# Kernel optimization log

Hardware: AMD Instinct MI355X
Metric: run time of the kernel (lower is better)

Reference implementation:

```python
import jax, jax.numpy as jnp
import numpy as np

EPS = 1e-5
G, N, H, P, K = 8, 128, 64, 64, 4  # n_groups, d_state, n_heads, head_dim, conv kernel
R = H // G  # heads per group


def _rmsnorm(x, w, eps=EPS):
    return x * jax.lax.rsqrt(jnp.mean(x * x, axis=-1, keepdims=True) + eps) * w


def setup_inputs() -> dict:
    key = jax.random.key(0)
    ks = jax.random.split(key, 8)
    B, L, Dm = 2, 1024, 2048
    d_inner = 2 * Dm                      # 4096
    conv_dim = d_inner + 2 * G * N        # 6144
    proj_dim = 2 * d_inner + 2 * G * N + H  # 10304
    return {
        "hidden_states": jax.random.normal(ks[0], (B, L, Dm), jnp.float32),
        "residual": jax.random.normal(ks[1], (B, L, Dm), jnp.float32),
        "norm_w": jnp.ones((Dm,), jnp.float32),
        "in_proj_w": jax.random.normal(ks[2], (proj_dim, Dm), jnp.float32) * 0.02,
        "conv_w": jax.random.normal(ks[3], (conv_dim, K), jnp.float32) * 0.1,
        "conv_b": jnp.zeros((conv_dim,), jnp.float32),
        "A_log": jnp.log(jnp.arange(1, H + 1, dtype=jnp.float32)),
        "D_param": jnp.ones((H,), jnp.float32),
        "dt_bias": jax.random.uniform(ks[4], (H,), jnp.float32, -4.0, -1.0),
        "gate_norm_w": jnp.ones((d_inner,), jnp.float32),
        "out_proj_w": jax.random.normal(ks[5], (Dm, d_inner), jnp.float32) * 0.02,
    }


def reference(hidden_states, residual, norm_w, in_proj_w, conv_w, conv_b,
              A_log, D_param, dt_bias, gate_norm_w, out_proj_w):
    B, L, Dm = hidden_states.shape
    d_inner = 2 * Dm
    conv_dim = d_inner + 2 * G * N

    # fused residual-add RMSNorm (residual is not None branch)
    h = hidden_states + residual
    new_residual = h
    x = _rmsnorm(h, norm_w)

    # in_proj -> [z | xBC | dt]
    proj = jnp.einsum('bld,ed->ble', x, in_proj_w)
    z = proj[..., :d_inner]
    xBC = proj[..., d_inner:d_inner + conv_dim]
    dt = proj[..., d_inner + conv_dim:]            # [B, L, H]

    # causal depthwise conv1d over xBC, then SiLU
    lhs = jnp.transpose(xBC, (0, 2, 1))            # [B, C, L]
    rhs = conv_w[:, None, :]                       # [C, 1, K]
    conv = jax.lax.conv_general_dilated(
        lhs, rhs, window_strides=(1,), padding=[(K - 1, 0)],
        feature_group_count=conv_dim)
    xBC = jax.nn.silu(jnp.transpose(conv, (0, 2, 1)) + conv_b)

    xs = xBC[..., :d_inner].reshape(B, L, G, R, P)   # per-head inputs
    Bm = xBC[..., d_inner:d_inner + G * N].reshape(B, L, G, N)
    Cm = xBC[..., d_inner + G * N:].reshape(B, L, G, N)

    dt = jax.nn.softplus(dt + dt_bias)               # [B, L, H]
    A = -jnp.exp(A_log)                              # [H]
    dA = jnp.exp(dt * A).reshape(B, L, G, R)
    dtg = dt.reshape(B, L, G, R)

    # time-major for scan
    def step(hst, inp):
        dA_t, dt_t, x_t, B_t, C_t = inp            # [B,G,R], [B,G,R], [B,G,R,P], [B,G,N], [B,G,N]
        dBx = jnp.einsum('bgr,bgn,bgrp->bgrpn', dt_t, B_t, x_t)
        hst = hst * dA_t[..., None, None] + dBx    # [B,G,R,P,N]
        y_t = jnp.einsum('bgrpn,bgn->bgrp', hst, C_t)
        return hst, y_t

    tm = lambda a: jnp.moveaxis(a, 1, 0)
    h0 = jnp.zeros((B, G, R, P, N), hidden_states.dtype)
    _, ys = jax.lax.scan(step, h0, (tm(dA), tm(dtg), tm(xs), tm(Bm), tm(Cm)))
    y = jnp.moveaxis(ys, 0, 1)                     # [B, L, G, R, P]
    y = y + D_param.reshape(G, R)[None, None, :, :, None] * xs
    y = y.reshape(B, L, d_inner)

    # gated RMSNorm then out_proj
    y = _rmsnorm(y * jax.nn.silu(z), gate_norm_w)
    out = jnp.einsum('ble,de->bld', y, out_proj_w)
    return out, new_residual
```

## Files before the change

kernel.cpp:

```cpp
#include <hip/hip_runtime.h>

#define TOK 2048
#define DM 2048
#define DI 4096
#define NG 8
#define NN 128
#define PROJ_D 10304
#define PROJ_P 10496
#define CONV_D 6144
#define LSEQ 1024
#define CHUNK 64
#define NCHUNK 16

typedef unsigned short u16;
typedef __attribute__((ext_vector_type(4))) float f32x4;
typedef __attribute__((ext_vector_type(8))) short s16x8;
typedef __attribute__((ext_vector_type(4))) unsigned short u16x4;

__device__ __forceinline__ u16 f2bf(float f) {
  union { float f; unsigned u; } x; x.f = f;
  unsigned r = (x.u + 0x7FFFu + ((x.u >> 16) & 1u)) >> 16;
  return (u16)r;
}
__device__ __forceinline__ float bf2f(u16 u) {
  union { unsigned u; float f; } x; x.u = ((unsigned)u) << 16; return x.f;
}

__device__ __forceinline__ float blockReduceSum256(float s) {
  __shared__ float red[4];
  #pragma unroll
  for (int o = 32; o > 0; o >>= 1) s += __shfl_down(s, o, 64);
  int lane = threadIdx.x & 63, wid = threadIdx.x >> 6;
  if (lane == 0) red[wid] = s;
  __syncthreads();
  return red[0] + red[1] + red[2] + red[3];
}

__global__ __launch_bounds__(256) void cvt_bf16_pad(const float* __restrict__ src, u16* __restrict__ dst,
                                                    long n_src, long n_dst) {
  long i = ((long)blockIdx.x * 256 + threadIdx.x) * 4;
  if (i >= n_dst) return;
  u16x4 o;
  if (i < n_src) {
    f32x4 v = *(const f32x4*)&src[i];
    o.x = f2bf(v.x); o.y = f2bf(v.y); o.z = f2bf(v.z); o.w = f2bf(v.w);
  } else {
    o.x = 0; o.y = 0; o.z = 0; o.w = 0;
  }
  *(u16x4*)&dst[i] = o;
}

__global__ __launch_bounds__(256) void addnorm_kernel(const float* __restrict__ hs, const float* __restrict__ res,
        const float* __restrict__ w, float* __restrict__ nres, u16* __restrict__ xbf) {
  int row = blockIdx.x;
  size_t base = (size_t)row * DM;
  int tid = threadIdx.x;
  f32x4 h[2];
  float s = 0.f;
  #pragma unroll
  for (int i = 0; i < 2; i++) {
    int off = i * 1024 + tid * 4;
    f32x4 a = *(const f32x4*)&hs[base + off];
    f32x4 b = *(const f32x4*)&res[base + off];
    f32x4 v = a + b;
    h[i] = v;
    *(f32x4*)&nres[base + off] = v;
    s += v.x * v.x + v.y * v.y + v.z * v.z + v.w * v.w;
  }
  s = blockReduceSum256(s);
  float rs = rsqrtf(s * (1.f / DM) + 1e-5f);
  #pragma unroll
  for (int i = 0; i < 2; i++) {
    int off = i * 1024 + tid * 4;
    f32x4 wv = *(const f32x4*)&w[off];
    f32x4 v = h[i];
    u16x4 o;
    o.x = f2bf(v.x * rs * wv.x);
    o.y = f2bf(v.y * rs * wv.y);
    o.z = f2bf(v.z * rs * wv.z);
    o.w = f2bf(v.w * rs * wv.w);
    *(u16x4*)&xbf[base + off] = o;
  }
}

__device__ __forceinline__ void gld_lds16(const void* g, void* l) {
  __builtin_amdgcn_global_load_lds((const __attribute__((address_space(1))) void*)g,
                                   (__attribute__((address_space(3))) void*)l, 16, 0, 0);
}

__global__ __launch_bounds__(512, 2) void gemm8p(const u16* __restrict__ A, const u16* __restrict__ Bw,
                                                 u16* __restrict__ C, int K, int Cstride, int nbx) {
  __shared__ u16 As[2][256][64];
  __shared__ u16 Bs[2][256][64];
  int tid = threadIdx.x;
  int lane = tid & 63, w = tid >> 6;
  int wr = w >> 2, wc = w & 3;
  int cpx = gridDim.x >> 3;
  int bid = blockIdx.x;
  int lb = (bid & 7) * cpx + (bid >> 3);
  int by = lb / nbx, bx = lb - by * nbx;
  size_t m0 = (size_t)by * 256, n0 = (size_t)bx * 256;
  const u16* Ab = A + m0 * K;
  const u16* Bb = Bw + n0 * K;

  f32x4 acc[8][4];
  #pragma unroll
  for (int i = 0; i < 8; ++i)
    #pragma unroll
    for (int j = 0; j < 4; ++j) acc[i][j] = (f32x4){0.f, 0.f, 0.f, 0.f};

  int l3 = lane >> 3;
  int colsw = ((lane & 7) ^ l3) << 3;
  int fr = lane & 15, fq = lane >> 4;
  int pc0 = (fq * 8) ^ ((fr & 7) << 3);
  int pc1 = pc0 ^ 32;

  auto S = [&](int kt, int mat, int half) {
    int d = kt & 1;
    const u16* src = mat ? Bb : Ab;
    u16* dstbase = mat ? &Bs[d][0][0] : &As[d][0][0];
    #pragma unroll
    for (int j = 0; j < 2; ++j) {
      int rb = half * 128 + (w * 2 + j) * 8;
      gld_lds16(src + (size_t)(rb + l3) * K + kt * 64 + colsw, dstbase + rb * 64);
    }
  };

  int nkt = K >> 6;
  S(0, 1, 0); S(0, 1, 1); S(0, 0, 0); S(0, 0, 1);
  S(1, 1, 0); S(1, 1, 1);
  asm volatile("s_waitcnt vmcnt(4)" ::: "memory");
  __builtin_amdgcn_s_barrier();

  for (int kt = 0; kt < nkt; ++kt) {
    int d = kt & 1;
    s16x8 b[4][2];
    #pragma unroll
    for (int q = 0; q < 4; ++q) {
      if (q == 0) {
        #pragma unroll
        for (int ni = 0; ni < 4; ++ni) {
          b[ni][0] = *(const s16x8*)&Bs[d][wc * 64 + ni * 16 + fr][pc0];
          b[ni][1] = *(const s16x8*)&Bs[d][wc * 64 + ni * 16 + fr][pc1];
        }
      }
      s16x8 a[2][2];
      #pragma unroll
      for (int mi = 0; mi < 2; ++mi) {
        a[mi][0] = *(const s16x8*)&As[d][wr * 128 + q * 32 + mi * 16 + fr][pc0];
        a[mi][1] = *(const s16x8*)&As[d][wr * 128 + q * 32 + mi * 16 + fr][pc1];
      }
      if (q == 0)      { if (kt + 1 < nkt) S(kt + 1, 0, 0); }
      else if (q == 1) { if (kt + 1 < nkt) S(kt + 1, 0, 1); }
      else if (q == 2) { if (kt + 2 < nkt) S(kt + 2, 1, 0); }
      else {
        if (kt + 2 < nkt) { S(kt + 2, 1, 1); asm volatile("s_waitcnt vmcnt(4)" ::: "memory"); }
        else              { asm volatile("s_waitcnt vmcnt(0)" ::: "memory"); }
      }
      __builtin_amdgcn_s_barrier();
      __builtin_amdgcn_s_setprio(1);
      #pragma unroll
      for (int mi = 0; mi < 2; ++mi)
        #pragma unroll
        for (int ni = 0; ni < 4; ++ni) {
          acc[q * 2 + mi][ni] = __builtin_amdgcn_mfma_f32_16x16x32_bf16(a[mi][0], b[ni][0], acc[q * 2 + mi][ni], 0, 0, 0);
          acc[q * 2 + mi][ni] = __builtin_amdgcn_mfma_f32_16x16x32_bf16(a[mi][1], b[ni][1], acc[q * 2 + mi][ni], 0, 0, 0);
        }
      __builtin_amdgcn_s_setprio(0);
      __builtin_amdgcn_s_barrier();
    }
  }
  size_t crow0 = m0 + wr * 128 + fq * 4;
  size_t ccol0 = n0 + wc * 64 + fr;
  #pragma unroll
  for (int mf = 0; mf < 8; ++mf)
    #pragma unroll
    for (int ni = 0; ni < 4; ++ni)
      #pragma unroll
      for (int j = 0; j < 4; ++j)
        C[(crow0 + mf * 16 + j) * Cstride + ccol0 + ni * 16] = f2bf(acc[mf][ni][j]);
}

template <int BM, int BN>
__global__ __launch_bounds__((BM / 64) * (BN / 64) * 64, 2)
void gemm_pipe(const u16* __restrict__ A, const u16* __restrict__ Bw,
               float* __restrict__ C, int K, int Cstride, int nbx) {
  constexpr int WM = BM / 64, WN = BN / 64;
  constexpr int NA = 8 / WN;
  constexpr int NB = 8 / WM;
  constexpr int NV = NA + NB;
  __shared__ u16 As[2][BM][64];
  __shared__ u16 Bs[2][BN][64];
  int tid = threadIdx.x;
  int lane = tid & 63, w = tid >> 6;
  int wr = w / WN, wc = w % WN;
  int cpx = gridDim.x >> 3;
  int bid = blockIdx.x;
  int lb = (bid & 7) * cpx + (bid >> 3);
  int by = lb / nbx, bx = lb - by * nbx;
  size_t m0 = (size_t)by * BM, n0 = (size_t)bx * BN;
  const u16* Ab = A + m0 * K;
  const u16* Bb = Bw + n0 * K;

  f32x4 acc[4][4];
  #pragma unroll
  for (int i = 0; i < 4; ++i)
    #pragma unroll
    for (int j = 0; j < 4; ++j) acc[i][j] = (f32x4){0.f, 0.f, 0.f, 0.f};

  int l3 = lane >> 3;
  int colsw = ((lane & 7) ^ l3) << 3;
  int fr = lane & 15, fq = lane >> 4;
  int pc0 = (fq * 8) ^ ((fr & 7) << 3);
  int pc1 = pc0 ^ 32;

  auto STAGE = [&](int d, int kt) {
    #pragma unroll
    for (int j = 0; j < NA; ++j) {
      int row = wr * 64 + (wc * NA + j) * 8;
      gld_lds16(Ab + (size_t)(row + l3) * K + kt * 64 + colsw, &As[d][row][0]);
    }
    #pragma unroll
    for (int j = 0; j < NB; ++j) {
      int row = wc * 64 + (wr * NB + j) * 8;
      gld_lds16(Bb + (size_t)(row + l3) * K + kt * 64 + colsw, &Bs[d][row][0]);
    }
  };

  int nkt = K >> 6;
  STAGE(0, 0);
  for (int kt = 0; kt < nkt; ++kt) {
    int d = kt & 1, nd = d ^ 1;
    if (kt + 1 < nkt) {
      STAGE(nd, kt + 1);
      if constexpr (NV == 6) asm volatile("s_waitcnt vmcnt(6)" ::: "memory");
      else                   asm volatile("s_waitcnt vmcnt(8)" ::: "memory");
    } else {
      asm volatile("s_waitcnt vmcnt(0)" ::: "memory");
    }
    __builtin_amdgcn_s_barrier();
    s16x8 b[4][2];
    #pragma unroll
    for (int ni = 0; ni < 4; ++ni) {
      b[ni][0] = *(const s16x8*)&Bs[d][wc * 64 + ni * 16 + fr][pc0];
      b[ni][1] = *(const s16x8*)&Bs[d][wc * 64 + ni * 16 + fr][pc1];
    }
    {
      s16x8 a[2][2];
      #pragma unroll
      for (int mi = 0; mi < 2; ++mi) {
        a[mi][0] = *(const s16x8*)&As[d][wr * 64 + mi * 16 + fr][pc0];
        a[mi][1] = *(const s16x8*)&As[d][wr * 64 + mi * 16 + fr][pc1];
      }
      __builtin_amdgcn_s_setprio(1);
      #pragma unroll
      for (int mi = 0; mi < 2; ++mi)
        #pragma unroll
        for (int ni = 0; ni < 4; ++ni) {
          acc[mi][ni] = __builtin_amdgcn_mfma_f32_16x16x32_bf16(a[mi][0], b[ni][0], acc[mi][ni], 0, 0, 0);
          acc[mi][ni] = __builtin_amdgcn_mfma_f32_16x16x32_bf16(a[mi][1], b[ni][1], acc[mi][ni], 0, 0, 0);
        }
      __builtin_amdgcn_s_setprio(0);
    }
    __builtin_amdgcn_s_barrier();
    {
      s16x8 a[2][2];
      #pragma unroll
      for (int mi = 0; mi < 2; ++mi) {
        a[mi][0] = *(const s16x8*)&As[d][wr * 64 + (mi + 2) * 16 + fr][pc0];
        a[mi][1] = *(const s16x8*)&As[d][wr * 64 + (mi + 2) * 16 + fr][pc1];
      }
      __builtin_amdgcn_s_setprio(1);
      #pragma unroll
      for (int mi = 0; mi < 2; ++mi)
        #pragma unroll
        for (int ni = 0; ni < 4; ++ni) {
          acc[mi + 2][ni] = __builtin_amdgcn_mfma_f32_16x16x32_bf16(a[mi][0], b[ni][0], acc[mi + 2][ni], 0, 0, 0);
          acc[mi + 2][ni] = __builtin_amdgcn_mfma_f32_16x16x32_bf16(a[mi][1], b[ni][1], acc[mi + 2][ni], 0, 0, 0);
        }
      __builtin_amdgcn_s_setprio(0);
    }
    __builtin_amdgcn_s_barrier();
  }
  size_t crow0 = m0 + wr * 64 + fq * 4;
  size_t ccol0 = n0 + wc * 64 + fr;
  #pragma unroll
  for (int mi = 0; mi < 4; ++mi)
    #pragma unroll
    for (int ni = 0; ni < 4; ++ni)
      #pragma unroll
      for (int j = 0; j < 4; ++j)
        C[(crow0 + mi * 16 + j) * Cstride + ccol0 + ni * 16] = acc[mi][ni][j];
}

__global__ __launch_bounds__(256) void conv_silu_kernel(const u16* __restrict__ proj,
        const float* __restrict__ cw, const float* __restrict__ cb, u16* __restrict__ xbc) {
  long gid = (long)blockIdx.x * 256 + threadIdx.x;
  int c4 = (int)(gid % 1536);
  long t = gid / 1536;
  int l = (int)(t & 1023);
  int c = c4 * 4;
  const u16* base = proj + (size_t)t * PROJ_P + DI + c;
  f32x4 acc = *(const f32x4*)&cb[c];
  f32x4 w0 = *(const f32x4*)&cw[(c + 0) * 4];
  f32x4 w1 = *(const f32x4*)&cw[(c + 1) * 4];
  f32x4 w2 = *(const f32x4*)&cw[(c + 2) * 4];
  f32x4 w3 = *(const f32x4*)&cw[(c + 3) * 4];
  #pragma unroll
  for (int k = 0; k < 4; k++) {
    int ls = l - 3 + k;
    if (ls >= 0) {
      u16x4 v = *(const u16x4*)(base + ((long)(k - 3)) * PROJ_P);
      acc.x = fmaf(bf2f(v.x), w0[k], acc.x);
      acc.y = fmaf(bf2f(v.y), w1[k], acc.y);
      acc.z = fmaf(bf2f(v.z), w2[k], acc.z);
      acc.w = fmaf(bf2f(v.w), w3[k], acc.w);
    }
  }
  u16x4 o;
  o.x = f2bf(acc.x / (1.f + expf(-acc.x)));
  o.y = f2bf(acc.y / (1.f + expf(-acc.y)));
  o.z = f2bf(acc.z / (1.f + expf(-acc.z)));
  o.w = f2bf(acc.w / (1.f + expf(-acc.w)));
  *(u16x4*)&xbc[(size_t)t * CONV_D + c] = o;
}

__global__ __launch_bounds__(256) void dt_kernel(const u16* __restrict__ proj, const float* __restrict__ dt_bias,
        const float* __restrict__ A_log, float* __restrict__ dtspT, float* __restrict__ dtaT) {
  int idx = blockIdx.x * 256 + threadIdx.x;
  int t = idx >> 6, hh = idx & 63;
  int b = t >> 10, l = t & 1023;
  float dtv = bf2f(proj[(size_t)t * PROJ_P + (DI + CONV_D) + hh]) + dt_bias[hh];
  float sp = (dtv > 15.f) ? dtv : log1pf(expf(dtv));
  float Ah = -expf(A_log[hh]);
  size_t o = (size_t)(b * 64 + hh) * LSEQ + l;
  dtspT[o] = sp;
  dtaT[o] = sp * Ah;
}

__global__ __launch_bounds__(512) void ssd_kernel(const u16* __restrict__ xbc, const float* __restrict__ dtsp,
        const float* __restrict__ dta, const float* __restrict__ Dp, float* __restrict__ y) {
  int bid = blockIdx.x;
  int g = bid & 7, b = (bid >> 3) & 1, r = bid >> 4;
  int h = g * 8 + r;
  int tid = threadIdx.x;
  int w = tid >> 6, lane = tid & 63;

  __shared__ u16 Bsh[2][64][128];
  __shared__ u16 Csh[2][64][128];
  __shared__ u16 Xt[2][64][64];
  __shared__ u16 Btw[2][128][64];
  __shared__ u16 GWsh[64][64];
  __shared__ u16 Hbf[64][128];
  __shared__ float dtsh[LSEQ];
  __shared__ float Lsh[LSEQ];

  const float* dtrow = dtsp + (size_t)(b * 64 + h) * LSEQ;
  const float* dtarow = dta + (size_t)(b * 64 + h) * LSEQ;
  if (tid < 256) { f32x4 v = *(const f32x4*)&dtrow[tid * 4]; *(f32x4*)&dtsh[tid * 4] = v; }
  for (int cc = w; cc < NCHUNK; cc += 8) {
    float a = dtarow[cc * 64 + lane];
    #pragma unroll
    for (int o = 1; o < 64; o <<= 1) { float t2 = __shfl_up(a, o, 64); if (lane >= o) a += t2; }
    Lsh[cc * 64 + lane] = a;
  }
  {
    u16* hp = &Hbf[0][0];
    for (int i = tid; i < 2048; i += 512) *(u16x4*)&hp[i * 4] = (u16x4){0, 0, 0, 0};
  }
  float Dv = Dp[h];
  const u16* xb = xbc + (size_t)b * LSEQ * CONV_D;
  int swz = (lane & 7) << 3;
  __syncthreads();

  auto stage = [&](int cc, int d) {
    int t0c = cc * 64;
    int pw = w - 4, ptid = tid - 256;
    #pragma unroll
    for (int q = 0; q < 4; ++q) {
      int rowb = pw * 16 + q * 4;
      int row = rowb + (lane >> 4);
      int colb = ((lane & 15) * 8) ^ ((row & 7) << 3);
      gld_lds16(xb + (size_t)(t0c + row) * CONV_D + DI + g * 128 + colb, &Bsh[d][rowb][0]);
      gld_lds16(xb + (size_t)(t0c + row) * CONV_D + DI + NG * NN + g * 128 + colb, &Csh[d][rowb][0]);
    }
    {
      int s = ptid & 63, pq = ptid >> 6;
      const u16* xr = xb + (size_t)(t0c + s) * CONV_D + g * 512 + r * 64;
      #pragma unroll
      for (int pb = 0; pb < 4; ++pb) {
        int p0 = pb * 16 + pq * 4;
        u16x4 v = *(const u16x4*)&xr[p0];
        #pragma unroll
        for (int j = 0; j < 4; ++j) {
          int p = p0 + j;
          Xt[d][p][s ^ ((p & 7) << 3)] = v[j];
        }
      }
    }
    {
      int s = ptid & 63, nq = ptid >> 6;
      float wend = __expf(Lsh[t0c + 63] - Lsh[t0c + s]) * dtsh[t0c + s];
      const u16* br = xb + (size_t)(t0c + s) * CONV_D + DI + g * 128;
      #pragma unroll
      for (int nb = 0; nb < 8; ++nb) {
        int n0 = nb * 16 + nq * 4;
        u16x4 v = *(const u16x4*)&br[n0];
        #pragma unroll
        for (int j = 0; j < 4; ++j) {
          int n = n0 + j;
          Btw[d][n][s ^ ((n & 7) << 3)] = f2bf(bf2f(v[j]) * wend);
        }
      }
    }
  };

  if (w >= 4) stage(0, 0);
  __syncthreads();

  f32x4 hst[8];
  #pragma unroll
  for (int i = 0; i < 8; i++) hst[i] = (f32x4){0.f, 0.f, 0.f, 0.f};

  for (int c = 0; c < NCHUNK; ++c) {
    int d = c & 1;
    int t0c = c * 64;
    f32x4 Yacc[4], Y2acc[4];
    s16x8 aC[4];
    float el[4];
    if (w >= 4) {
      if (c + 1 < NCHUNK) stage(c + 1, d ^ 1);
    } else {
      #pragma unroll
      for (int k = 0; k < 4; ++k)
        aC[k] = *(const s16x8*)&Csh[d][w * 16 + (lane & 15)][(k * 32 + (lane >> 4) * 8) ^ swz];
      f32x4 Gacc[4];
      #pragma unroll
      for (int st = 0; st < 4; ++st) Gacc[st] = (f32x4){0.f, 0.f, 0.f, 0.f};
      #pragma unroll
      for (int st = 0; st < 4; ++st)
        #pragma unroll
        for (int k = 0; k < 4; ++k) {
          s16x8 bB = *(const s16x8*)&Bsh[d][st * 16 + (lane & 15)][(k * 32 + (lane >> 4) * 8) ^ swz];
          Gacc[st] = __builtin_amdgcn_mfma_f32_16x16x32_bf16(aC[k], bB, Gacc[st], 0, 0, 0);
        }
      #pragma unroll
      for (int st = 0; st < 4; ++st) {
        int s = st * 16 + (lane & 15);
        float Ls = Lsh[t0c + s], dts = dtsh[t0c + s];
        #pragma unroll
        for (int j = 0; j < 4; ++j) {
          int t = w * 16 + (lane >> 4) * 4 + j;
          float wgt = (s <= t) ? __expf(Lsh[t0c + t] - Ls) * dts : 0.f;
          GWsh[t][s ^ ((t & 7) << 3)] = f2bf(Gacc[st][j] * wgt);
        }
      }
      #pragma unroll
      for (int pt = 0; pt < 4; ++pt) { Yacc[pt] = (f32x4){0.f,0.f,0.f,0.f}; Y2acc[pt] = (f32x4){0.f,0.f,0.f,0.f}; }
      s16x8 aGW[2];
      #pragma unroll
      for (int k = 0; k < 2; ++k)
        aGW[k] = *(const s16x8*)&GWsh[w * 16 + (lane & 15)][(k * 32 + (lane >> 4) * 8) ^ swz];
      #pragma unroll
      for (int pt = 0; pt < 4; ++pt) {
        #pragma unroll
        for (int k = 0; k < 2; ++k) {
          s16x8 bX = *(const s16x8*)&Xt[d][pt * 16 + (lane & 15)][(k * 32 + (lane >> 4) * 8) ^ swz];
          Yacc[pt] = __builtin_amdgcn_mfma_f32_16x16x32_bf16(aGW[k], bX, Yacc[pt], 0, 0, 0);
        }
        #pragma unroll
        for (int k = 0; k < 4; ++k) {
          s16x8 bH = *(const s16x8*)&Hbf[pt * 16 + (lane & 15)][(k * 32 + (lane >> 4) * 8) ^ swz];
          Y2acc[pt] = __builtin_amdgcn_mfma_f32_16x16x32_bf16(aC[k], bH, Y2acc[pt], 0, 0, 0);
        }
      }
      #pragma unroll
      for (int j = 0; j < 4; ++j) el[j] = __expf(Lsh[t0c + w * 16 + (lane >> 4) * 4 + j]);
      #pragma unroll
      for (int pt = 0; pt < 4; ++pt) {
        int p = pt * 16 + (lane & 15);
        #pragma unroll
        for (int j = 0; j < 4; ++j) {
          int t = w * 16 + (lane >> 4) * 4 + j;
          float xv = bf2f(Xt[d][p][t ^ ((p & 7) << 3)]);
          float yv = Yacc[pt][j] + el[j] * Y2acc[pt][j] + Dv * xv;
          y[((size_t)b * LSEQ + t0c + t) * DI + g * 512 + r * 64 + p] = yv;
        }
      }
      float e63 = __expf(Lsh[t0c + 63]);
      s16x8 aX[2];
      #pragma unroll
      for (int k = 0; k < 2; ++k)
        aX[k] = *(const s16x8*)&Xt[d][w * 16 + (lane & 15)][(k * 32 + (lane >> 4) * 8) ^ swz];
      #pragma unroll
      for (int nt = 0; nt < 8; ++nt) {
        #pragma unroll
        for (int j = 0; j < 4; ++j) hst[nt][j] *= e63;
        #pragma unroll
        for (int k = 0; k < 2; ++k) {
          s16x8 bW = *(const s16x8*)&Btw[d][nt * 16 + (lane & 15)][(k * 32 + (lane >> 4) * 8) ^ swz];
          hst[nt] = __builtin_amdgcn_mfma_f32_16x16x32_bf16(aX[k], bW, hst[nt], 0, 0, 0);
        }
      }
    }
    __syncthreads();
    if (w < 4) {
      #pragma unroll
      for (int nt = 0; nt < 8; ++nt) {
        int n = nt * 16 + (lane & 15);
        #pragma unroll
        for (int j = 0; j < 4; ++j) {
          int p = w * 16 + (lane >> 4) * 4 + j;
          Hbf[p][n ^ ((p & 7) << 3)] = f2bf(hst[nt][j]);
        }
      }
    }
    __syncthreads();
  }
}

__global__ __launch_bounds__(256) void gate_kernel(const float* __restrict__ y, const u16* __restrict__ proj,
        const float* __restrict__ gw, u16* __restrict__ y2) {
  int row = blockIdx.x;
  const float* yr = y + (size_t)row * DI;
  const u16* zr = proj + (size_t)row * PROJ_P;
  int tid = threadIdx.x;
  f32x4 v[4];
  float s = 0.f;
  #pragma unroll
  for (int i = 0; i < 4; i++) {
    int off = i * 1024 + tid * 4;
    f32x4 a = *(const f32x4*)&yr[off];
    u16x4 zv = *(const u16x4*)&zr[off];
    f32x4 t;
    float z0 = bf2f(zv.x), z1 = bf2f(zv.y), z2 = bf2f(zv.z), z3 = bf2f(zv.w);
    t.x = a.x * (z0 / (1.f + expf(-z0)));
    t.y = a.y * (z1 / (1.f + expf(-z1)));
    t.z = a.z * (z2 / (1.f + expf(-z2)));
    t.w = a.w * (z3 / (1.f + expf(-z3)));
    v[i] = t;
    s += t.x * t.x + t.y * t.y + t.z * t.z + t.w * t.w;
  }
  s = blockReduceSum256(s);
  float rs = rsqrtf(s * (1.f / DI) + 1e-5f);
  #pragma unroll
  for (int i = 0; i < 4; i++) {
    int off = i * 1024 + tid * 4;
    f32x4 wv = *(const f32x4*)&gw[off];
    u16x4 o;
    o.x = f2bf(v[i].x * rs * wv.x);
    o.y = f2bf(v[i].y * rs * wv.y);
    o.z = f2bf(v[i].z * rs * wv.z);
    o.w = f2bf(v[i].w * rs * wv.w);
    *(u16x4*)&y2[(size_t)row * DI + off] = o;
  }
}

extern "C" void kernel_launch(void* const* d_in, const int* in_sizes, int n_in,
                              void* d_out, int out_size, void* d_ws, size_t ws_size,
                              hipStream_t stream) {
  (void)in_sizes; (void)n_in; (void)out_size; (void)ws_size;
  const float* hs      = (const float*)d_in[0];
  const float* res     = (const float*)d_in[1];
  const float* norm_w  = (const float*)d_in[2];
  const float* w_in    = (const float*)d_in[3];
  const float* conv_w  = (const float*)d_in[4];
  const float* conv_b  = (const float*)d_in[5];
  const float* A_log   = (const float*)d_in[6];
  const float* D_param = (const float*)d_in[7];
  const float* dt_bias = (const float*)d_in[8];
  const float* gate_w  = (const float*)d_in[9];
  const float* w_out   = (const float*)d_in[10];

  float* out  = (float*)d_out;
  float* nres = out + (size_t)TOK * DM;

  char* ws = (char*)d_ws;
  size_t off = 0;
  u16*   WB1  = (u16*)(ws + off);   off += (size_t)PROJ_P * DM * 2;
  u16*   WB2  = (u16*)(ws + off);   off += (size_t)DM * DI * 2;
  u16*   XBF  = (u16*)(ws + off);   off += (size_t)TOK * DM * 2;
  u16*   PROJ = (u16*)(ws + off);   off += (size_t)TOK * PROJ_P * 2;
  u16*   XBC  = (u16*)(ws + off);   off += (size_t)TOK * CONV_D * 2;
  float* DTSP = (float*)(ws + off); off += (size_t)TOK * 64 * 4;
  float* DTA  = (float*)(ws + off); off += (size_t)TOK * 64 * 4;
  float* Y    = (float*)(ws + off); off += (size_t)TOK * DI * 4;
  u16*   Y2   = (u16*)(ws + off);   off += (size_t)TOK * DI * 2;

  cvt_bf16_pad<<<20992, 256, 0, stream>>>(w_in, WB1, (long)PROJ_D * DM, (long)PROJ_P * DM);
  cvt_bf16_pad<<<8192, 256, 0, stream>>>(w_out, WB2, (long)DM * DI, (long)DM * DI);
  addnorm_kernel<<<TOK, 256, 0, stream>>>(hs, res, norm_w, nres, XBF);
  gemm8p<<<(TOK / 256) * (PROJ_P / 256), 512, 0, stream>>>(XBF, WB1, PROJ, DM, PROJ_P, PROJ_P / 256);
  conv_silu_kernel<<<(TOK * (CONV_D / 4)) / 256, 256, 0, stream>>>(PROJ, conv_w, conv_b, XBC);
  dt_kernel<<<(TOK * 64) / 256, 256, 0, stream>>>(PROJ, dt_bias, A_log, DTSP, DTA);
  ssd_kernel<<<128, 512, 0, stream>>>(XBC, DTSP, DTA, D_param, Y);
  gate_kernel<<<TOK, 256, 0, stream>>>(Y, PROJ, gate_w, Y2);
  gemm_pipe<128, 128><<<(TOK / 128) * (DM / 128), 256, 0, stream>>>(Y2, WB2, out, DI, DM, DM / 128);
}
```

Before: 336.9 us.

## Use split-K 256x256 GEMM for out_proj and store SSD output as bf16

The out_proj GEMM moves from the 128x128 gemm_pipe kernel to the 256x256 gemm8p kernel with a 4-way split-K. Each split writes an fp32 partial, and a new reduce kernel sums the four partials, which keeps 256 blocks in flight instead of 64 large tiles. Separately, the SSD kernel writes y as bf16 instead of fp32, halving the traffic into the gate kernel. The cost is 64MB of extra partial-sum writes and reads plus one more launch, and some precision loss on y. There is also a stray, unused gemm8p_bf declaration.

```diff
diff --git a/kernel.cpp b/kernel.cpp
--- a/kernel.cpp
+++ b/kernel.cpp
@@ -88,8 +88,12 @@
                                    (__attribute__((address_space(3))) void*)l, 16, 0, 0);
 }
 
+__global__ __launch_bounds__(512, 2) void gemm8p_bf(const u16* __restrict__ A, const u16* __restrict__ Bw,
+                                                    u16* __restrict__ C, int K, int Cstride, int nbx);
+template <bool BF16OUT>
 __global__ __launch_bounds__(512, 2) void gemm8p(const u16* __restrict__ A, const u16* __restrict__ Bw,
-                                                 u16* __restrict__ C, int K, int Cstride, int nbx) {
+                                                 void* __restrict__ Cv, int K, int Cstride, int nbx,
+                                                 int nks, size_t part_stride) {
   __shared__ u16 As[2][256][64];
   __shared__ u16 Bs[2][256][64];
   int tid = threadIdx.x;
@@ -98,7 +102,11 @@
   int cpx = gridDim.x >> 3;
   int bid = blockIdx.x;
   int lb = (bid & 7) * cpx + (bid >> 3);
-  int by = lb / nbx, bx = lb - by * nbx;
+  int ks = lb % nks;
+  int tile = lb / nks;
+  int by = tile / nbx, bx = tile - by * nbx;
+  int Ks = K / nks;
+  int k0 = ks * Ks;
   size_t m0 = (size_t)by * 256, n0 = (size_t)bx * 256;
   const u16* Ab = A + m0 * K;
   const u16* Bb = Bw + n0 * K;
@@ -122,11 +130,11 @@
     #pragma unroll
     for (int j = 0; j < 2; ++j) {
       int rb = half * 128 + (w * 2 + j) * 8;
-      gld_lds16(src + (size_t)(rb + l3) * K + kt * 64 + colsw, dstbase + rb * 64);
+      gld_lds16(src + (size_t)(rb + l3) * K + k0 + kt * 64 + colsw, dstbase + rb * 64);
     }
   };
 
-  int nkt = K >> 6;
+  int nkt = Ks >> 6;
   S(0, 1, 0); S(0, 1, 1); S(0, 0, 0); S(0, 0, 1);
   S(1, 1, 0); S(1, 1, 1);
   asm volatile("s_waitcnt vmcnt(4)" ::: "memory");
@@ -172,125 +180,35 @@
   }
   size_t crow0 = m0 + wr * 128 + fq * 4;
   size_t ccol0 = n0 + wc * 64 + fr;
-  #pragma unroll
-  for (int mf = 0; mf < 8; ++mf)
-    #pragma unroll
-    for (int ni = 0; ni < 4; ++ni)
-      #pragma unroll
-      for (int j = 0; j < 4; ++j)
-        C[(crow0 + mf * 16 + j) * Cstride + ccol0 + ni * 16] = f2bf(acc[mf][ni][j]);
-}
-
-template <int BM, int BN>
-__global__ __launch_bounds__((BM / 64) * (BN / 64) * 64, 2)
-void gemm_pipe(const u16* __restrict__ A, const u16* __restrict__ Bw,
-               float* __restrict__ C, int K, int Cstride, int nbx) {
-  constexpr int WM = BM / 64, WN = BN / 64;
-  constexpr int NA = 8 / WN;
-  constexpr int NB = 8 / WM;
-  constexpr int NV = NA + NB;
-  __shared__ u16 As[2][BM][64];
-  __shared__ u16 Bs[2][BN][64];
-  int tid = threadIdx.x;
-  int lane = tid & 63, w = tid >> 6;
-  int wr = w / WN, wc = w % WN;
-  int cpx = gridDim.x >> 3;
-  int bid = blockIdx.x;
-  int lb = (bid & 7) * cpx + (bid >> 3);
-  int by = lb / nbx, bx = lb - by * nbx;
-  size_t m0 = (size_t)by * BM, n0 = (size_t)bx * BN;
-  const u16* Ab = A + m0 * K;
-  const u16* Bb = Bw + n0 * K;
-
-  f32x4 acc[4][4];
-  #pragma unroll
-  for (int i = 0; i < 4; ++i)
-    #pragma unroll
-    for (int j = 0; j < 4; ++j) acc[i][j] = (f32x4){0.f, 0.f, 0.f, 0.f};
-
-  int l3 = lane >> 3;
-  int colsw = ((lane & 7) ^ l3) << 3;
-  int fr = lane & 15, fq = lane >> 4;
-  int pc0 = (fq * 8) ^ ((fr & 7) << 3);
-  int pc1 = pc0 ^ 32;
-
-  auto STAGE = [&](int d, int kt) {
-    #pragma unroll
-    for (int j = 0; j < NA; ++j) {
-      int row = wr * 64 + (wc * NA + j) * 8;
-      gld_lds16(Ab + (size_t)(row + l3) * K + kt * 64 + colsw, &As[d][row][0]);
-    }
-    #pragma unroll
-    for (int j = 0; j < NB; ++j) {
-      int row = wc * 64 + (wr * NB + j) * 8;
-      gld_lds16(Bb + (size_t)(row + l3) * K + kt * 64 + colsw, &Bs[d][row][0]);
-    }
-  };
-
-  int nkt = K >> 6;
-  STAGE(0, 0);
-  for (int kt = 0; kt < nkt; ++kt) {
-    int d = kt & 1, nd = d ^ 1;
-    if (kt + 1 < nkt) {
-      STAGE(nd, kt + 1);
-      if constexpr (NV == 6) asm volatile("s_waitcnt vmcnt(6)" ::: "memory");
-      else                   asm volatile("s_waitcnt vmcnt(8)" ::: "memory");
-    } else {
-      asm volatile("s_waitcnt vmcnt(0)" ::: "memory");
-    }
-    __builtin_amdgcn_s_barrier();
-    s16x8 b[4][2];
-    #pragma unroll
-    for (int ni = 0; ni < 4; ++ni) {
-      b[ni][0] = *(const s16x8*)&Bs[d][wc * 64 + ni * 16 + fr][pc0];
-      b[ni][1] = *(const s16x8*)&Bs[d][wc * 64 + ni * 16 + fr][pc1];
-    }
-    {
-      s16x8 a[2][2];
-      #pragma unroll
-      for (int mi = 0; mi < 2; ++mi) {
-        a[mi][0] = *(const s16x8*)&As[d][wr * 64 + mi * 16 + fr][pc0];
-        a[mi][1] = *(const s16x8*)&As[d][wr * 64 + mi * 16 + fr][pc1];
-      }
-      __builtin_amdgcn_s_setprio(1);
-      #pragma unroll
-      for (int mi = 0; mi < 2; ++mi)
-        #pragma unroll
-        for (int ni = 0; ni < 4; ++ni) {
-          acc[mi][ni] = __builtin_amdgcn_mfma_f32_16x16x32_bf16(a[mi][0], b[ni][0], acc[mi][ni], 0, 0, 0);
-          acc[mi][ni] = __builtin_amdgcn_mfma_f32_16x16x32_bf16(a[mi][1], b[ni][1], acc[mi][ni], 0, 0, 0);
-        }
-      __builtin_amdgcn_s_setprio(0);
-    }
-    __builtin_amdgcn_s_barrier();
-    {
-      s16x8 a[2][2];
-      #pragma unroll
-      for (int mi = 0; mi < 2; ++mi) {
-        a[mi][0] = *(const s16x8*)&As[d][wr * 64 + (mi + 2) * 16 + fr][pc0];
-        a[mi][1] = *(const s16x8*)&As[d][wr * 64 + (mi + 2) * 16 + fr][pc1];
-      }
-      __builtin_amdgcn_s_setprio(1);
-      #pragma unroll
-      for (int mi = 0; mi < 2; ++mi)
-        #pragma unroll
-        for (int ni = 0; ni < 4; ++ni) {
-          acc[mi + 2][ni] = __builtin_amdgcn_mfma_f32_16x16x32_bf16(a[mi][0], b[ni][0], acc[mi + 2][ni], 0, 0, 0);
-          acc[mi + 2][ni] = __builtin_amdgcn_mfma_f32_16x16x32_bf16(a[mi][1], b[ni][1], acc[mi + 2][ni], 0, 0, 0);
-        }
-      __builtin_amdgcn_s_setprio(0);
-    }
-    __builtin_amdgcn_s_barrier();
-  }
-  size_t crow0 = m0 + wr * 64 + fq * 4;
-  size_t ccol0 = n0 + wc * 64 + fr;
-  #pragma unroll
-  for (int mi = 0; mi < 4; ++mi)
-    #pragma unroll
-    for (int ni = 0; ni < 4; ++ni)
-      #pragma unroll
-      for (int j = 0; j < 4; ++j)
-        C[(crow0 + mi * 16 + j) * Cstride + ccol0 + ni * 16] = acc[mi][ni][j];
+  if constexpr (BF16OUT) {
+    u16* C = (u16*)Cv;
+    #pragma unroll
+    for (int mf = 0; mf < 8; ++mf)
+      #pragma unroll
+      for (int ni = 0; ni < 4; ++ni)
+        #pragma unroll
+        for (int j = 0; j < 4; ++j)
+          C[(crow0 + mf * 16 + j) * Cstride + ccol0 + ni * 16] = f2bf(acc[mf][ni][j]);
+  } else {
+    float* C = (float*)Cv + (size_t)ks * part_stride;
+    #pragma unroll
+    for (int mf = 0; mf < 8; ++mf)
+      #pragma unroll
+      for (int ni = 0; ni < 4; ++ni)
+        #pragma unroll
+        for (int j = 0; j < 4; ++j)
+          C[(crow0 + mf * 16 + j) * Cstride + ccol0 + ni * 16] = acc[mf][ni][j];
+  }
+}
+
+__global__ __launch_bounds__(256) void reduce4_kernel(const float* __restrict__ part, float* __restrict__ out) {
+  size_t i = ((size_t)blockIdx.x * 256 + threadIdx.x) * 4;
+  const size_t st = (size_t)TOK * DM;
+  f32x4 s = *(const f32x4*)&part[i];
+  s += *(const f32x4*)&part[i + st];
+  s += *(const f32x4*)&part[i + 2 * st];
+  s += *(const f32x4*)&part[i + 3 * st];
+  *(f32x4*)&out[i] = s;
 }
 
 __global__ __launch_bounds__(256) void conv_silu_kernel(const u16* __restrict__ proj,
@@ -339,7 +257,7 @@
 }
 
 __global__ __launch_bounds__(512) void ssd_kernel(const u16* __restrict__ xbc, const float* __restrict__ dtsp,
-        const float* __restrict__ dta, const float* __restrict__ Dp, float* __restrict__ y) {
+        const float* __restrict__ dta, const float* __restrict__ Dp, u16* __restrict__ y) {
   int bid = blockIdx.x;
   int g = bid & 7, b = (bid >> 3) & 1, r = bid >> 4;
   int h = g * 8 + r;
@@ -425,12 +343,10 @@
   for (int c = 0; c < NCHUNK; ++c) {
     int d = c & 1;
     int t0c = c * 64;
-    f32x4 Yacc[4], Y2acc[4];
-    s16x8 aC[4];
-    float el[4];
     if (w >= 4) {
       if (c + 1 < NCHUNK) stage(c + 1, d ^ 1);
     } else {
+      s16x8 aC[4];
       #pragma unroll
       for (int k = 0; k < 4; ++k)
         aC[k] = *(const s16x8*)&Csh[d][w * 16 + (lane & 15)][(k * 32 + (lane >> 4) * 8) ^ swz];
@@ -455,6 +371,7 @@
           GWsh[t][s ^ ((t & 7) << 3)] = f2bf(Gacc[st][j] * wgt);
         }
       }
+      f32x4 Yacc[4], Y2acc[4];
       #pragma unroll
       for (int pt = 0; pt < 4; ++pt) { Yacc[pt] = (f32x4){0.f,0.f,0.f,0.f}; Y2acc[pt] = (f32x4){0.f,0.f,0.f,0.f}; }
       s16x8 aGW[2];
@@ -474,6 +391,7 @@
           Y2acc[pt] = __builtin_amdgcn_mfma_f32_16x16x32_bf16(aC[k], bH, Y2acc[pt], 0, 0, 0);
         }
       }
+      float el[4];
       #pragma unroll
       for (int j = 0; j < 4; ++j) el[j] = __expf(Lsh[t0c + w * 16 + (lane >> 4) * 4 + j]);
       #pragma unroll
@@ -484,7 +402,7 @@
           int t = w * 16 + (lane >> 4) * 4 + j;
           float xv = bf2f(Xt[d][p][t ^ ((p & 7) << 3)]);
           float yv = Yacc[pt][j] + el[j] * Y2acc[pt][j] + Dv * xv;
-          y[((size_t)b * LSEQ + t0c + t) * DI + g * 512 + r * 64 + p] = yv;
+          y[((size_t)b * LSEQ + t0c + t) * DI + g * 512 + r * 64 + p] = f2bf(yv);
         }
       }
       float e63 = __expf(Lsh[t0c + 63]);
@@ -519,10 +437,10 @@
   }
 }
 
-__global__ __launch_bounds__(256) void gate_kernel(const float* __restrict__ y, const u16* __restrict__ proj,
+__global__ __launch_bounds__(256) void gate_kernel(const u16* __restrict__ y, const u16* __restrict__ proj,
         const float* __restrict__ gw, u16* __restrict__ y2) {
   int row = blockIdx.x;
-  const float* yr = y + (size_t)row * DI;
+  const u16* yr = y + (size_t)row * DI;
   const u16* zr = proj + (size_t)row * PROJ_P;
   int tid = threadIdx.x;
   f32x4 v[4];
@@ -530,14 +448,14 @@
   #pragma unroll
   for (int i = 0; i < 4; i++) {
     int off = i * 1024 + tid * 4;
-    f32x4 a = *(const f32x4*)&yr[off];
+    u16x4 av = *(const u16x4*)&yr[off];
     u16x4 zv = *(const u16x4*)&zr[off];
     f32x4 t;
     float z0 = bf2f(zv.x), z1 = bf2f(zv.y), z2 = bf2f(zv.z), z3 = bf2f(zv.w);
-    t.x = a.x * (z0 / (1.f + expf(-z0)));
-    t.y = a.y * (z1 / (1.f + expf(-z1)));
-    t.z = a.z * (z2 / (1.f + expf(-z2)));
-    t.w = a.w * (z3 / (1.f + expf(-z3)));
+    t.x = bf2f(av.x) * (z0 / (1.f + expf(-z0)));
+    t.y = bf2f(av.y) * (z1 / (1.f + expf(-z1)));
+    t.z = bf2f(av.z) * (z2 / (1.f + expf(-z2)));
+    t.w = bf2f(av.w) * (z3 / (1.f + expf(-z3)));
     v[i] = t;
     s += t.x * t.x + t.y * t.y + t.z * t.z + t.w * t.w;
   }
@@ -584,16 +502,18 @@
   u16*   XBC  = (u16*)(ws + off);   off += (size_t)TOK * CONV_D * 2;
   float* DTSP = (float*)(ws + off); off += (size_t)TOK * 64 * 4;
   float* DTA  = (float*)(ws + off); off += (size_t)TOK * 64 * 4;
-  float* Y    = (float*)(ws + off); off += (size_t)TOK * DI * 4;
+  u16*   Y    = (u16*)(ws + off);   off += (size_t)TOK * DI * 2;
   u16*   Y2   = (u16*)(ws + off);   off += (size_t)TOK * DI * 2;
+  float* PART = (float*)(ws + off); off += (size_t)4 * TOK * DM * 4;
 
   cvt_bf16_pad<<<20992, 256, 0, stream>>>(w_in, WB1, (long)PROJ_D * DM, (long)PROJ_P * DM);
   cvt_bf16_pad<<<8192, 256, 0, stream>>>(w_out, WB2, (long)DM * DI, (long)DM * DI);
   addnorm_kernel<<<TOK, 256, 0, stream>>>(hs, res, norm_w, nres, XBF);
-  gemm8p<<<(TOK / 256) * (PROJ_P / 256), 512, 0, stream>>>(XBF, WB1, PROJ, DM, PROJ_P, PROJ_P / 256);
+  gemm8p<true><<<(TOK / 256) * (PROJ_P / 256), 512, 0, stream>>>(XBF, WB1, PROJ, DM, PROJ_P, PROJ_P / 256, 1, 0);
   conv_silu_kernel<<<(TOK * (CONV_D / 4)) / 256, 256, 0, stream>>>(PROJ, conv_w, conv_b, XBC);
   dt_kernel<<<(TOK * 64) / 256, 256, 0, stream>>>(PROJ, dt_bias, A_log, DTSP, DTA);
   ssd_kernel<<<128, 512, 0, stream>>>(XBC, DTSP, DTA, D_param, Y);
   gate_kernel<<<TOK, 256, 0, stream>>>(Y, PROJ, gate_w, Y2);
-  gemm_pipe<128, 128><<<(TOK / 128) * (DM / 128), 256, 0, stream>>>(Y2, WB2, out, DI, DM, DM / 128);
-}
+  gemm8p<false><<<(TOK / 256) * (DM / 256) * 4, 512, 0, stream>>>(Y2, WB2, PART, DI, DM, DM / 256, 4, (size_t)TOK * DM);
+  reduce4_kernel<<<(TOK * DM) / 1024, 256, 0, stream>>>(PART, out);
+}
```

Result: faster. 325.7 us (-3.4%).
